# Optimization experiments

Measured on AMD Instinct MI355X. Metric: run time of the kernel, lower is better.

Reference implementation:

```python
import jax, jax.numpy as jnp
import numpy as np

NUM_COND = 16  # num_conditions
EPS = 1e-5


def setup_inputs() -> dict:
    key = jax.random.key(0)
    k1, k2, k3, k4 = jax.random.split(key, 4)
    N, F = 500000, 128
    x = jax.random.normal(k1, (N, F), dtype=jnp.float32)
    labels = jax.random.randint(k2, (N,), 0, NUM_COND)
    gamma = jax.random.uniform(k3, (NUM_COND, F), dtype=jnp.float32)
    beta = jax.random.normal(k4, (NUM_COND, F), dtype=jnp.float32)
    return {"x": x, "labels": labels, "gamma": gamma, "beta": beta}


def reference(x, labels, gamma, beta):
    # Conditional BatchNorm1d (training mode): per-label batch statistics
    # over the samples of each group, then per-label affine transform.
    num_cond = gamma.shape[0]
    ones = jnp.ones((x.shape[0],), x.dtype)
    counts = jax.ops.segment_sum(ones, labels, num_segments=num_cond)   # [C]
    counts = jnp.maximum(counts, 1.0)                                    # guard empty groups
    s1 = jax.ops.segment_sum(x, labels, num_segments=num_cond)          # [C,F]
    s2 = jax.ops.segment_sum(x * x, labels, num_segments=num_cond)      # [C,F]
    mean = s1 / counts[:, None]
    var = s2 / counts[:, None] - mean * mean                             # biased var (BatchNorm)
    inv_std = jax.lax.rsqrt(var + EPS)                                   # [C,F]
    scale = gamma * inv_std                                              # [C,F]
    shift = beta - mean * scale                                          # [C,F]
    y = x * scale[labels] + shift[labels]                                # fused gather + affine
    return y
```

## Files before the change

### kernel.cpp

```cpp
#include <hip/hip_runtime.h>

#define NUM_COND 16
#define FDIM 128
#define EPS 1e-5f
#define WPB 4
#define PB 4160
#define NCHUNK 16
#define MAXNB 512

typedef float __attribute__((ext_vector_type(4))) f4v;
__device__ __forceinline__ void nt_store4(float4* p, const float4& v) {
    f4v t = { v.x, v.y, v.z, v.w };
    __builtin_nontemporal_store(t, (f4v*)p);
}

__global__ __launch_bounds__(256) void cbn_stats_kernel(
    const float* __restrict__ x, const int* __restrict__ labels,
    float* __restrict__ ws, int N, int Npairs, int pchunk)
{
    __shared__ float acc[WPB][4096];
    const int t = threadIdx.x;
    const int w = t >> 6;
    const int lane = t & 63;
    const int half = lane >> 5;
    const int sl = lane & 31;

    {
        float4* z = (float4*)acc[w];
        for (int i = lane; i < 1024; i += 64) z[i] = make_float4(0.f, 0.f, 0.f, 0.f);
    }

    const int pbeg = blockIdx.x * pchunk;
    const int pend = min(Npairs, pbeg + pchunk);
    const float4* x4 = (const float4*)x;
    float4* r1 = (float4*)acc[w];
    float4* r2 = r1 + 512;

    int cnt = 0;
    float4 v0, v1, v2, v3;
    int lb0 = 0, lb1 = 0, lb2 = 0, lb3 = 0;
    int row0 = N, row1 = N, row2 = N, row3 = N;
    v0 = v1 = v2 = v3 = make_float4(0.f, 0.f, 0.f, 0.f);

#define LOADSLOT(S, P)                                              \
    {   const int p_ = (P);                                         \
        if (p_ < pend) {                                            \
            row##S = 2 * p_ + half;                                 \
            const int rc_ = min(row##S, N - 1);                     \
            v##S = x4[(size_t)rc_ * 32 + sl];                       \
            lb##S = labels[rc_];                                    \
        }                                                           \
    }

#define PROCSLOT(S, P)                                              \
    {   const int p_ = (P);                                         \
        if (p_ < pend && row##S < N) {                              \
            const int o_ = lb##S * 32 + sl;                         \
            float4 a = r1[o_];                                      \
            float4 b = r2[o_];                                      \
            a.x += v##S.x; a.y += v##S.y;                           \
            a.z += v##S.z; a.w += v##S.w;                           \
            b.x = fmaf(v##S.x, v##S.x, b.x);                        \
            b.y = fmaf(v##S.y, v##S.y, b.y);                        \
            b.z = fmaf(v##S.z, v##S.z, b.z);                        \
            b.w = fmaf(v##S.w, v##S.w, b.w);                        \
            r1[o_] = a;                                             \
            r2[o_] = b;                                             \
            cnt += ((lane & 15) == lb##S) ? 1 : 0;                  \
        }                                                           \
    }

    int p = pbeg + w;
    LOADSLOT(0, p)
    LOADSLOT(1, p + WPB)
    LOADSLOT(2, p + 2 * WPB)
    LOADSLOT(3, p + 3 * WPB)

    for (; p < pend; p += 4 * WPB) {
        PROCSLOT(0, p)
        LOADSLOT(0, p + 4 * WPB)
        PROCSLOT(1, p + WPB)
        LOADSLOT(1, p + 5 * WPB)
        PROCSLOT(2, p + 2 * WPB)
        LOADSLOT(2, p + 6 * WPB)
        PROCSLOT(3, p + 3 * WPB)
        LOADSLOT(3, p + 7 * WPB)
    }

    __syncthreads();
    float* out = ws + (size_t)blockIdx.x * PB;
    for (int i = t; i < 4096; i += 256)
        out[i] = acc[0][i] + acc[1][i] + acc[2][i] + acc[3][i];
    const int c2 = cnt + __shfl(cnt, lane ^ 32);
    if (lane < 16) out[4096 + w * 16 + lane] = (float)c2;
}

__global__ __launch_bounds__(256) void cbn_reduce_kernel(
    const float* __restrict__ ws, float* __restrict__ ws2, int nb, int per)
{
    const int e = blockIdx.x * 256 + threadIdx.x;
    if (e >= PB) return;
    const int b0 = blockIdx.y * per;
    const int b1 = min(nb, b0 + per);
    float a = 0.f;
#pragma unroll 8
    for (int b = b0; b < b1; ++b) a += ws[(size_t)b * PB + e];
    ws2[(size_t)blockIdx.y * PB + e] = a;
}

__global__ __launch_bounds__(256) void cbn_finalize_kernel(
    const float* __restrict__ ws2, const float* __restrict__ gamma,
    const float* __restrict__ beta, float* __restrict__ scale_shift)
{
    const int e = blockIdx.x * 256 + threadIdx.x;
    const int lab = e >> 7;
    float a1 = 0.f, a2 = 0.f, cn = 0.f;
#pragma unroll
    for (int k = 0; k < NCHUNK; ++k) {
        const float* p = ws2 + (size_t)k * PB;
        a1 += p[e];
        a2 += p[2048 + e];
#pragma unroll
        for (int w2 = 0; w2 < WPB; ++w2)
            cn += p[4096 + w2 * 16 + lab];
    }
    cn = fmaxf(cn, 1.0f);
    const float mean = a1 / cn;
    const float var  = a2 / cn - mean * mean;
    const float sc = gamma[e] * rsqrtf(var + EPS);
    const float sh = beta[e] - mean * sc;
    scale_shift[e]        = sc;
    scale_shift[2048 + e] = sh;
}

__global__ __launch_bounds__(256) void cbn_apply_kernel(
    const float* __restrict__ x, const int* __restrict__ labels,
    const float* __restrict__ scale_shift, float* __restrict__ y, int N)
{
    __shared__ float4 ssc[NUM_COND * 32];
    __shared__ float4 ssh[NUM_COND * 32];
    const int t = threadIdx.x;
    const float4* ss4 = (const float4*)scale_shift;
    for (int i = t; i < NUM_COND * 32; i += 256) {
        ssc[i] = ss4[i];
        ssh[i] = ss4[512 + i];
    }
    __syncthreads();

    const int f4 = t & 31;
    const int rg = t >> 5;
    const float4* x4 = (const float4*)x;
    float4* y4 = (float4*)y;

    for (int base = blockIdx.x * 32 + rg; base < N; base += gridDim.x * 32) {
        const int r0 = base;
        int r1 = base + 8, r2 = base + 16, r3 = base + 24;
        const bool k1 = r1 < N, k2 = r2 < N, k3 = r3 < N;
        if (!k1) r1 = r0;  if (!k2) r2 = r0;  if (!k3) r3 = r0;

        const int l0 = labels[r0], l1 = labels[r1], l2 = labels[r2], l3 = labels[r3];
        const float4 v0 = x4[(size_t)r0 * 32 + f4];
        const float4 v1 = x4[(size_t)r1 * 32 + f4];
        const float4 v2 = x4[(size_t)r2 * 32 + f4];
        const float4 v3 = x4[(size_t)r3 * 32 + f4];

        const float4 c0 = ssc[l0 * 32 + f4], h0 = ssh[l0 * 32 + f4];
        const float4 c1 = ssc[l1 * 32 + f4], h1 = ssh[l1 * 32 + f4];
        const float4 c2 = ssc[l2 * 32 + f4], h2 = ssh[l2 * 32 + f4];
        const float4 c3 = ssc[l3 * 32 + f4], h3 = ssh[l3 * 32 + f4];

        float4 o0, o1, o2, o3;
        o0.x = fmaf(v0.x, c0.x, h0.x); o0.y = fmaf(v0.y, c0.y, h0.y);
        o0.z = fmaf(v0.z, c0.z, h0.z); o0.w = fmaf(v0.w, c0.w, h0.w);
        o1.x = fmaf(v1.x, c1.x, h1.x); o1.y = fmaf(v1.y, c1.y, h1.y);
        o1.z = fmaf(v1.z, c1.z, h1.z); o1.w = fmaf(v1.w, c1.w, h1.w);
        o2.x = fmaf(v2.x, c2.x, h2.x); o2.y = fmaf(v2.y, c2.y, h2.y);
        o2.z = fmaf(v2.z, c2.z, h2.z); o2.w = fmaf(v2.w, c2.w, h2.w);
        o3.x = fmaf(v3.x, c3.x, h3.x); o3.y = fmaf(v3.y, c3.y, h3.y);
        o3.z = fmaf(v3.z, c3.z, h3.z); o3.w = fmaf(v3.w, c3.w, h3.w);

        nt_store4(&y4[(size_t)r0 * 32 + f4], o0);
        if (k1) nt_store4(&y4[(size_t)r1 * 32 + f4], o1);
        if (k2) nt_store4(&y4[(size_t)r2 * 32 + f4], o2);
        if (k3) nt_store4(&y4[(size_t)r3 * 32 + f4], o3);
    }
}

extern "C" void kernel_launch(void* const* d_in, const int* in_sizes, int n_in,
                              void* d_out, int out_size, void* d_ws, size_t ws_size,
                              hipStream_t stream)
{
    const float* x      = (const float*)d_in[0];
    const int*   labels = (const int*)d_in[1];
    const float* gamma  = (const float*)d_in[2];
    const float* beta   = (const float*)d_in[3];
    float* y  = (float*)d_out;
    float* ws = (float*)d_ws;
    const int N = in_sizes[1];
    const int Npairs = (N + 1) / 2;

    const long floats = (long)(ws_size / sizeof(float));
    long avail = floats - (long)NCHUNK * PB - 4096;
    int nb = MAXNB;
    if ((long)nb * PB > avail) nb = (int)(avail / PB);
    if (nb < 1) nb = 1;
    const int pchunk = (Npairs + nb - 1) / nb;
    const int per    = (nb + NCHUNK - 1) / NCHUNK;

    float* ws2         = ws + (size_t)nb * PB;
    float* scale_shift = ws2 + (size_t)NCHUNK * PB;

    cbn_stats_kernel<<<nb, 256, 0, stream>>>(x, labels, ws, N, Npairs, pchunk);
    cbn_reduce_kernel<<<dim3((PB + 255) / 256, NCHUNK), 256, 0, stream>>>(ws, ws2, nb, per);
    cbn_finalize_kernel<<<8, 256, 0, stream>>>(ws2, gamma, beta, scale_shift);
    cbn_apply_kernel<<<2048, 256, 0, stream>>>(x, labels, scale_shift, y, N);
}
```

Measured before the change: 157.0 us.

## Transpose row pairs through LDS staging so stats RMW uses one label per wave

The stats kernel now writes each wave's two loaded rows into a small LDS staging buffer. It reads them back as float2, so each read-modify-write of the per-label accumulators covers a single row, and therefore a single label, across all 64 lanes. Before, the two half-waves could update different label rows with float4 accesses. Blocks shrink to two waves (128 threads), the pipelining depth goes from four slots to three, and the block count limit doubles to 1024. The extra LDS round trip adds instructions, and more blocks means more partial sums for the reduce kernel to add up.

```diff
diff --git a/kernel.cpp b/kernel.cpp
--- a/kernel.cpp
+++ b/kernel.cpp
@@ -3,10 +3,11 @@
 #define NUM_COND 16
 #define FDIM 128
 #define EPS 1e-5f
-#define WPB 4
+#define WPB 2
+#define NSLOT 3
 #define PB 4160
 #define NCHUNK 16
-#define MAXNB 512
+#define MAXNB 1024
 
 typedef float __attribute__((ext_vector_type(4))) f4v;
 __device__ __forceinline__ void nt_store4(float4* p, const float4& v) {
@@ -14,11 +15,12 @@
     __builtin_nontemporal_store(t, (f4v*)p);
 }
 
-__global__ __launch_bounds__(256) void cbn_stats_kernel(
+__global__ __launch_bounds__(128) void cbn_stats_kernel(
     const float* __restrict__ x, const int* __restrict__ labels,
     float* __restrict__ ws, int N, int Npairs, int pchunk)
 {
     __shared__ float acc[WPB][4096];
+    __shared__ float stage[WPB][NSLOT * 256];
     const int t = threadIdx.x;
     const int w = t >> 6;
     const int lane = t & 63;
@@ -33,66 +35,67 @@
     const int pbeg = blockIdx.x * pchunk;
     const int pend = min(Npairs, pbeg + pchunk);
     const float4* x4 = (const float4*)x;
-    float4* r1 = (float4*)acc[w];
-    float4* r2 = r1 + 512;
+    float2* r1 = (float2*)acc[w];
+    float2* r2 = r1 + 1024;
+    float4* stg4 = (float4*)stage[w];
+    float2* stg2 = (float2*)stage[w];
 
     int cnt = 0;
-    float4 v0, v1, v2, v3;
-    int lb0 = 0, lb1 = 0, lb2 = 0, lb3 = 0;
-    int row0 = N, row1 = N, row2 = N, row3 = N;
-    v0 = v1 = v2 = v3 = make_float4(0.f, 0.f, 0.f, 0.f);
-
-#define LOADSLOT(S, P)                                              \
-    {   const int p_ = (P);                                         \
-        if (p_ < pend) {                                            \
-            row##S = 2 * p_ + half;                                 \
-            const int rc_ = min(row##S, N - 1);                     \
-            v##S = x4[(size_t)rc_ * 32 + sl];                       \
-            lb##S = labels[rc_];                                    \
-        }                                                           \
-    }
-
-#define PROCSLOT(S, P)                                              \
-    {   const int p_ = (P);                                         \
-        if (p_ < pend && row##S < N) {                              \
-            const int o_ = lb##S * 32 + sl;                         \
-            float4 a = r1[o_];                                      \
-            float4 b = r2[o_];                                      \
-            a.x += v##S.x; a.y += v##S.y;                           \
-            a.z += v##S.z; a.w += v##S.w;                           \
-            b.x = fmaf(v##S.x, v##S.x, b.x);                        \
-            b.y = fmaf(v##S.y, v##S.y, b.y);                        \
-            b.z = fmaf(v##S.z, v##S.z, b.z);                        \
-            b.w = fmaf(v##S.w, v##S.w, b.w);                        \
-            r1[o_] = a;                                             \
-            r2[o_] = b;                                             \
-            cnt += ((lane & 15) == lb##S) ? 1 : 0;                  \
-        }                                                           \
+    float4 v0, v1, v2;
+    int la0 = 0, la1 = 0, la2 = 0, lb0 = 0, lb1 = 0, lb2 = 0;
+    v0 = v1 = v2 = make_float4(0.f, 0.f, 0.f, 0.f);
+
+#define LOADSLOT(S, P)                                                  \
+    {   const int p_ = (P);                                             \
+        if (p_ < pend) {                                                \
+            const int r_ = min(2 * p_ + half, N - 1);                   \
+            v##S = x4[(size_t)r_ * 32 + sl];                            \
+            la##S = labels[2 * p_];                                     \
+            lb##S = labels[min(2 * p_ + 1, N - 1)];                     \
+        }                                                               \
+    }
+
+#define RMW(D, LB)                                                      \
+    {   const int o_ = (LB) * 64 + lane;                                \
+        float2 a_ = r1[o_];                                             \
+        float2 b_ = r2[o_];                                             \
+        a_.x += (D).x;                 a_.y += (D).y;                   \
+        b_.x = fmaf((D).x, (D).x, b_.x);                                \
+        b_.y = fmaf((D).y, (D).y, b_.y);                                \
+        r1[o_] = a_;                                                    \
+        r2[o_] = b_;                                                    \
+        cnt += ((lane & 15) == (LB)) ? 1 : 0;                           \
+    }
+
+#define PROCSLOT(S, P)                                                  \
+    {   const int p_ = (P);                                             \
+        if (p_ < pend) {                                                \
+            stg4[S * 64 + lane] = v##S;                                 \
+            { float2 d_ = stg2[S * 128 + lane];        RMW(d_, la##S) } \
+            if (2 * p_ + 1 < N) {                                       \
+              float2 d_ = stg2[S * 128 + 64 + lane];   RMW(d_, lb##S) } \
+        }                                                               \
     }
 
     int p = pbeg + w;
     LOADSLOT(0, p)
     LOADSLOT(1, p + WPB)
     LOADSLOT(2, p + 2 * WPB)
-    LOADSLOT(3, p + 3 * WPB)
-
-    for (; p < pend; p += 4 * WPB) {
+
+    for (; p < pend; p += NSLOT * WPB) {
         PROCSLOT(0, p)
-        LOADSLOT(0, p + 4 * WPB)
+        LOADSLOT(0, p + 3 * WPB)
         PROCSLOT(1, p + WPB)
-        LOADSLOT(1, p + 5 * WPB)
+        LOADSLOT(1, p + 4 * WPB)
         PROCSLOT(2, p + 2 * WPB)
-        LOADSLOT(2, p + 6 * WPB)
-        PROCSLOT(3, p + 3 * WPB)
-        LOADSLOT(3, p + 7 * WPB)
+        LOADSLOT(2, p + 5 * WPB)
     }
 
     __syncthreads();
     float* out = ws + (size_t)blockIdx.x * PB;
-    for (int i = t; i < 4096; i += 256)
-        out[i] = acc[0][i] + acc[1][i] + acc[2][i] + acc[3][i];
-    const int c2 = cnt + __shfl(cnt, lane ^ 32);
-    if (lane < 16) out[4096 + w * 16 + lane] = (float)c2;
+    for (int i = t; i < 4096; i += 128)
+        out[i] = acc[0][i] + acc[1][i];
+    if (lane < 16) out[4096 + w * 16 + lane] = (float)cnt;
 }
 
 __global__ __launch_bounds__(256) void cbn_reduce_kernel(
@@ -210,7 +213,7 @@
     float* ws2         = ws + (size_t)nb * PB;
     float* scale_shift = ws2 + (size_t)NCHUNK * PB;
 
-    cbn_stats_kernel<<<nb, 256, 0, stream>>>(x, labels, ws, N, Npairs, pchunk);
+    cbn_stats_kernel<<<nb, 128, 0, stream>>>(x, labels, ws, N, Npairs, pchunk);
     cbn_reduce_kernel<<<dim3((PB + 255) / 256, NCHUNK), 256, 0, stream>>>(ws, ws2, nb, per);
     cbn_finalize_kernel<<<8, 256, 0, stream>>>(ws2, gamma, beta, scale_shift);
     cbn_apply_kernel<<<2048, 256, 0, stream>>>(x, labels, scale_shift, y, N);
```

New measurement: 160.7 us. 1.02x slower.
